# Performance work log

Measured on AMD Instinct MI355X. Metric: run time of the kernel, lower is better.

Reference implementation:

```python
import jax, jax.numpy as jnp
import numpy as np

N_NODES = 50000
N_EDGES = 800000
IN_DIM, HID_DIM, OUT_DIM = 256, 256, 128


def setup_inputs() -> dict:
    key = jax.random.key(0)
    ks = jax.random.split(key, 8)
    x1 = jax.random.normal(ks[0], (N_NODES, IN_DIM), dtype=jnp.float32)
    x2 = jax.random.normal(ks[1], (N_NODES, IN_DIM), dtype=jnp.float32)
    edge_index1 = jax.random.randint(ks[2], (2, N_EDGES), 0, N_NODES, dtype=jnp.int32)
    edge_index2 = jax.random.randint(ks[3], (2, N_EDGES), 0, N_NODES, dtype=jnp.int32)
    # GCNConv weights (Glorot-ish scaling)
    W1 = jax.random.normal(ks[4], (IN_DIM, HID_DIM), dtype=jnp.float32) / np.sqrt(IN_DIM)
    b1 = jnp.zeros((HID_DIM,), dtype=jnp.float32)
    W2 = jax.random.normal(ks[5], (HID_DIM, OUT_DIM), dtype=jnp.float32) / np.sqrt(HID_DIM)
    b2 = jnp.zeros((OUT_DIM,), dtype=jnp.float32)
    return {"x1": x1, "edge_index1": edge_index1, "x2": x2, "edge_index2": edge_index2,
            "W1": W1, "b1": b1, "W2": W2, "b2": b2}


def gcn_conv(x, src, dst, W, b, n_nodes):
    """PyG GCNConv: h = x @ W; symmetric-normalized scatter-add with self-loops; + bias."""
    h = x @ W  # [N, D_out]
    loop = jnp.arange(n_nodes, dtype=src.dtype)
    s = jnp.concatenate([src, loop])  # [E+N]
    d = jnp.concatenate([dst, loop])
    deg = jax.ops.segment_sum(jnp.ones_like(d, dtype=h.dtype), d, num_segments=n_nodes)
    dinv = jax.lax.rsqrt(jnp.maximum(deg, 1.0))  # deg >= 1 with self-loops
    norm = dinv[s] * dinv[d]  # [E+N]
    msg = h[s] * norm[:, None]  # [E+N, D_out]
    out = jax.ops.segment_sum(msg, d, num_segments=n_nodes)
    return out + b


def gcn_backbone(x, edge_index, W1, b1, W2, b2):
    src, dst = edge_index[0], edge_index[1]
    n = x.shape[0]
    h = jax.nn.relu(gcn_conv(x, src, dst, W1, b1, n))
    return gcn_conv(h, src, dst, W2, b2, n)


def reference(x1, edge_index1, x2, edge_index2, W1, b1, W2, b2):
    u = gcn_backbone(x1, edge_index1, W1, b1, W2, b2)
    v = gcn_backbone(x2, edge_index2, W1, b1, W2, b2)
    return (u, v)
```

## Files before the change

### kernel.cpp

```cpp
#include <hip/hip_runtime.h>

typedef __bf16 bf16x8 __attribute__((ext_vector_type(8)));
typedef float f32x4 __attribute__((ext_vector_type(4)));

constexpr int NN = 50000;
constexpr int NE = 800000;
constexpr int DIN = 256, DHID = 256, DOUT = 128;
constexpr int NCH = (NN + 255) / 256;

__device__ __forceinline__ unsigned short f2bf(float f) {
  unsigned u = __float_as_uint(f);
  u += 0x7fffu + ((u >> 16) & 1u);
  return (unsigned short)(u >> 16);
}
__device__ __forceinline__ float bf2f(unsigned short h) {
  return __uint_as_float(((unsigned)h) << 16);
}


__global__ void hist_kernel(const int* __restrict__ e0, const int* __restrict__ e1,
                            int* __restrict__ counts) {
  int g = blockIdx.y;
  const int* dst = (g ? e1 : e0) + NE;
  int* c = counts + g * NN;
  int i = blockIdx.x * blockDim.x + threadIdx.x;
  if (i < NE) atomicAdd(&c[dst[i]], 1);
}


__global__ __launch_bounds__(256) void scanA_kernel(const int* __restrict__ counts,
                                                    int* __restrict__ bsum) {
  int g = blockIdx.y, chunk = blockIdx.x, t = threadIdx.x;
  int i = chunk * 256 + t;
  int v = (i < NN) ? counts[g * NN + i] : 0;
  __shared__ int sh[256];
  sh[t] = v;
  __syncthreads();
  for (int off = 128; off > 0; off >>= 1) {
    if (t < off) sh[t] += sh[t + off];
    __syncthreads();
  }
  if (t == 0) bsum[g * NCH + chunk] = sh[0];
}

__global__ __launch_bounds__(256) void scanB_kernel(int* __restrict__ bsum,
                                                    int* __restrict__ rowptr) {
  int g = blockIdx.x, t = threadIdx.x;
  int v = (t < NCH) ? bsum[g * NCH + t] : 0;
  __shared__ int sh[256];
  sh[t] = v;
  __syncthreads();
  for (int off = 1; off < 256; off <<= 1) {
    int x = (t >= off) ? sh[t - off] : 0;
    __syncthreads();
    if (t >= off) sh[t] += x;
    __syncthreads();
  }
  if (t < NCH) bsum[g * NCH + t] = sh[t] - v;
  if (t == 255) rowptr[g * (NN + 1) + NN] = sh[255];
}

__global__ __launch_bounds__(256) void scanC_kernel(const int* __restrict__ counts,
                                                    const int* __restrict__ bsum,
                                                    int* __restrict__ rowptr,
                                                    int* __restrict__ cursor,
                                                    float* __restrict__ dinv) {
  int g = blockIdx.y, chunk = blockIdx.x, t = threadIdx.x;
  int i = chunk * 256 + t;
  int v = (i < NN) ? counts[g * NN + i] : 0;
  __shared__ int sh[256];
  sh[t] = v;
  __syncthreads();
  for (int off = 1; off < 256; off <<= 1) {
    int x = (t >= off) ? sh[t - off] : 0;
    __syncthreads();
    if (t >= off) sh[t] += x;
    __syncthreads();
  }
  if (i < NN) {
    int run = bsum[g * NCH + chunk] + sh[t] - v;
    rowptr[g * (NN + 1) + i] = run;
    cursor[g * NN + i] = run;
    dinv[g * NN + i] = rsqrtf((float)(v + 1));
  }
}

__global__ void scatter_kernel(const int* __restrict__ e0, const int* __restrict__ e1,
                               int* __restrict__ cursor, unsigned short* __restrict__ col) {
  int g = blockIdx.y;
  const int* e = g ? e1 : e0;
  int* cur = cursor + g * NN;
  unsigned short* cl = col + g * NE;
  int i = blockIdx.x * blockDim.x + threadIdx.x;
  if (i < NE) {
    int s = e[i], d = e[NE + i];
    int slot = atomicAdd(&cur[d], 1);
    cl[slot] = (unsigned short)s;
  }
}


__global__ void pack_kernel(const float* __restrict__ W1, const float* __restrict__ W2,
                            unsigned short* __restrict__ P1, unsigned short* __restrict__ P2) {
  int i = blockIdx.x * blockDim.x + threadIdx.x;
  constexpr int N1 = 8 * 16 * 64 * 8;
  constexpr int N2 = 8 * 8 * 64 * 8;
  if (i < N1) {
    int j = i & 7, lane = (i >> 3) & 63, grp = i >> 9;
    int nt = grp & 15, kb = grp >> 4;
    int k = kb * 32 + (lane >> 4) * 8 + j;
    int n = nt * 16 + (lane & 15);
    P1[i] = f2bf(W1[k * DHID + n]);
  } else if (i < N1 + N2) {
    int ii = i - N1;
    int j = ii & 7, lane = (ii >> 3) & 63, grp = ii >> 9;
    int nt = grp & 7, kb = grp >> 3;
    int k = kb * 32 + (lane >> 4) * 8 + j;
    int n = nt * 16 + (lane & 15);
    P2[ii] = f2bf(W2[k * DOUT + n]);
  }
}


template <int N, bool AF32>
__global__ __launch_bounds__(256) void mm_kernel(
    const void* __restrict__ A0, const void* __restrict__ A1,
    const unsigned short* __restrict__ Wp, unsigned short* __restrict__ Cb,
    const float* __restrict__ dinv, long long gstride) {
  constexpr int NT = N / 16;
  constexpr int K = 256;
  int g = blockIdx.y;
  const void* A = g ? A1 : A0;
  unsigned short* C = Cb + (size_t)g * gstride;
  const float* dv = dinv + g * NN;
  int wave = threadIdx.x >> 6, lane = threadIdx.x & 63;
  int q = lane >> 4, lm = lane & 15;
  int m0 = blockIdx.x * 64 + wave * 16;
  int row = m0 + lm;
  int rowc = min(row, NN - 1);
  f32x4 acc[NT];
#pragma unroll
  for (int nt = 0; nt < NT; nt++) acc[nt] = (f32x4){0.f, 0.f, 0.f, 0.f};
#pragma unroll
  for (int kb = 0; kb < K / 32; kb++) {
    int kc = kb * 32 + q * 8;
    bf16x8 a;
    if constexpr (AF32) {
      const float* Af = (const float*)A + (size_t)rowc * K + kc;
      const float4 v0 = *(const float4*)Af;
      const float4 v1 = *(const float4*)(Af + 4);
      a[0] = (__bf16)v0.x; a[1] = (__bf16)v0.y; a[2] = (__bf16)v0.z; a[3] = (__bf16)v0.w;
      a[4] = (__bf16)v1.x; a[5] = (__bf16)v1.y; a[6] = (__bf16)v1.z; a[7] = (__bf16)v1.w;
    } else {
      const unsigned short* Ab = (const unsigned short*)A + (size_t)rowc * K + kc;
      a = *(const bf16x8*)Ab;
    }
#pragma unroll
    for (int nt = 0; nt < NT; nt++) {
      bf16x8 b = *(const bf16x8*)(Wp + (((size_t)kb * NT + nt) * 64 + lane) * 8);
      acc[nt] = __builtin_amdgcn_mfma_f32_16x16x32_bf16(a, b, acc[nt], 0, 0, 0);
    }
  }
  float dvr[4];
#pragma unroll
  for (int r = 0; r < 4; r++) dvr[r] = dv[min(m0 + q * 4 + r, NN - 1)];
#pragma unroll
  for (int nt = 0; nt < NT; nt++) {
#pragma unroll
    for (int r = 0; r < 4; r++) {
      int grow = m0 + q * 4 + r;
      if (grow < NN) C[(size_t)grow * N + nt * 16 + lm] = f2bf(acc[nt][r] * dvr[r]);
    }
  }
}


__global__ __launch_bounds__(256) void agg1_kernel(
    const unsigned short* __restrict__ m1, unsigned short* __restrict__ a1,
    const int* __restrict__ rowptr, const unsigned short* __restrict__ col,
    const float* __restrict__ dinv, const float* __restrict__ b1) {
  int g = blockIdx.y;
  const unsigned short* H = m1 + (size_t)g * NN * DHID;
  unsigned short* O = a1 + (size_t)g * NN * DHID;
  const int* rp = rowptr + g * (NN + 1);
  const unsigned short* cl = col + (size_t)g * NE;
  const float* dv = dinv + g * NN;
  int node = blockIdx.x * 4 + (threadIdx.x >> 6);
  if (node >= NN) return;
  int lane = threadIdx.x & 63;
  ushort4 sv = *(const ushort4*)(H + (size_t)node * DHID + lane * 4);
  float a0 = bf2f(sv.x), a1v = bf2f(sv.y), a2 = bf2f(sv.z), a3 = bf2f(sv.w);
  int jb = rp[node], je = rp[node + 1];
  int j = jb;
  for (; j + 16 <= je; j += 16) {
    int s[16];
    ushort4 v[16];
#pragma unroll
    for (int u = 0; u < 16; u++) s[u] = cl[j + u];
#pragma unroll
    for (int u = 0; u < 16; u++) v[u] = *(const ushort4*)(H + (size_t)s[u] * DHID + lane * 4);
#pragma unroll
    for (int u = 0; u < 16; u++) {
      a0 += bf2f(v[u].x); a1v += bf2f(v[u].y);
      a2 += bf2f(v[u].z); a3 += bf2f(v[u].w);
    }
  }
  for (; j + 8 <= je; j += 8) {
    int s[8];
    ushort4 v[8];
#pragma unroll
    for (int u = 0; u < 8; u++) s[u] = cl[j + u];
#pragma unroll
    for (int u = 0; u < 8; u++) v[u] = *(const ushort4*)(H + (size_t)s[u] * DHID + lane * 4);
#pragma unroll
    for (int u = 0; u < 8; u++) {
      a0 += bf2f(v[u].x); a1v += bf2f(v[u].y);
      a2 += bf2f(v[u].z); a3 += bf2f(v[u].w);
    }
  }
  for (; j < je; j++) {
    int s = cl[j];
    ushort4 hv = *(const ushort4*)(H + (size_t)s * DHID + lane * 4);
    a0 += bf2f(hv.x); a1v += bf2f(hv.y);
    a2 += bf2f(hv.z); a3 += bf2f(hv.w);
  }
  float di = dv[node];
  float4 bb = *(const float4*)(b1 + lane * 4);
  a0 = fmaxf(fmaf(a0, di, bb.x), 0.f); a1v = fmaxf(fmaf(a1v, di, bb.y), 0.f);
  a2 = fmaxf(fmaf(a2, di, bb.z), 0.f); a3 = fmaxf(fmaf(a3, di, bb.w), 0.f);
  ushort4 out;
  out.x = f2bf(a0); out.y = f2bf(a1v); out.z = f2bf(a2); out.w = f2bf(a3);
  *(ushort4*)(O + (size_t)node * DHID + lane * 4) = out;
}


__global__ __launch_bounds__(256) void agg2_kernel(
    const unsigned short* __restrict__ m2, float* __restrict__ out,
    const int* __restrict__ rowptr, const unsigned short* __restrict__ col,
    const float* __restrict__ dinv, const float* __restrict__ b2) {
  int g = blockIdx.y;
  const unsigned short* H = m2 + (size_t)g * NN * DHID;
  float* O = out + (size_t)g * NN * DOUT;
  const int* rp = rowptr + g * (NN + 1);
  const unsigned short* cl = col + (size_t)g * NE;
  const float* dv = dinv + g * NN;
  int node = blockIdx.x * 4 + (threadIdx.x >> 6);
  if (node >= NN) return;
  int lane = threadIdx.x & 63;
  ushort2 sv = *(const ushort2*)(H + (size_t)node * DOUT + lane * 2);
  float a0 = bf2f(sv.x), a1v = bf2f(sv.y);
  int jb = rp[node], je = rp[node + 1];
  int j = jb;
  for (; j + 16 <= je; j += 16) {
    int s[16];
    ushort2 v[16];
#pragma unroll
    for (int u = 0; u < 16; u++) s[u] = cl[j + u];
#pragma unroll
    for (int u = 0; u < 16; u++) v[u] = *(const ushort2*)(H + (size_t)s[u] * DOUT + lane * 2);
#pragma unroll
    for (int u = 0; u < 16; u++) { a0 += bf2f(v[u].x); a1v += bf2f(v[u].y); }
  }
  for (; j + 8 <= je; j += 8) {
    int s[8];
    ushort2 v[8];
#pragma unroll
    for (int u = 0; u < 8; u++) s[u] = cl[j + u];
#pragma unroll
    for (int u = 0; u < 8; u++) v[u] = *(const ushort2*)(H + (size_t)s[u] * DOUT + lane * 2);
#pragma unroll
    for (int u = 0; u < 8; u++) { a0 += bf2f(v[u].x); a1v += bf2f(v[u].y); }
  }
  for (; j < je; j++) {
    int s = cl[j];
    ushort2 hv = *(const ushort2*)(H + (size_t)s * DOUT + lane * 2);
    a0 += bf2f(hv.x); a1v += bf2f(hv.y);
  }
  float di = dv[node];
  float2 bb = *(const float2*)(b2 + lane * 2);
  float2 res;
  res.x = fmaf(a0, di, bb.x); res.y = fmaf(a1v, di, bb.y);
  *(float2*)(O + (size_t)node * DOUT + lane * 2) = res;
}


extern "C" void kernel_launch(void* const* d_in, const int* in_sizes, int n_in,
                              void* d_out, int out_size, void* d_ws, size_t ws_size,
                              hipStream_t stream) {
  const float* x1 = (const float*)d_in[0];
  const int* e1 = (const int*)d_in[1];
  const float* x2 = (const float*)d_in[2];
  const int* e2 = (const int*)d_in[3];
  const float* W1 = (const float*)d_in[4];
  const float* b1 = (const float*)d_in[5];
  const float* W2 = (const float*)d_in[6];
  const float* b2 = (const float*)d_in[7];
  float* out = (float*)d_out;

  char* base = (char*)d_ws;
  size_t off = 0;
  auto alloc = [&](size_t bytes) -> void* {
    void* p = base + off;
    off = (off + bytes + 511) & ~(size_t)511;
    return p;
  };
  int* counts = (int*)alloc((size_t)2 * NN * 4);
  int* rowptr = (int*)alloc((size_t)2 * (NN + 1) * 4);
  int* cursor = (int*)alloc((size_t)2 * NN * 4);
  float* dinv = (float*)alloc((size_t)2 * NN * 4);
  int* bsum = (int*)alloc((size_t)2 * NCH * 4);
  unsigned short* col = (unsigned short*)alloc((size_t)2 * NE * 2);
  unsigned short* m1 = (unsigned short*)alloc((size_t)2 * NN * DHID * 2);
  unsigned short* a1 = (unsigned short*)alloc((size_t)2 * NN * DHID * 2);
  unsigned short* P1 = (unsigned short*)alloc((size_t)8 * 16 * 64 * 8 * 2);
  unsigned short* P2 = (unsigned short*)alloc((size_t)8 * 8 * 64 * 8 * 2);

  hipMemsetAsync(counts, 0, (size_t)2 * NN * 4, stream);
  hist_kernel<<<dim3((NE + 255) / 256, 2), 256, 0, stream>>>(e1, e2, counts);
  scanA_kernel<<<dim3(NCH, 2), 256, 0, stream>>>(counts, bsum);
  scanB_kernel<<<2, 256, 0, stream>>>(bsum, rowptr);
  scanC_kernel<<<dim3(NCH, 2), 256, 0, stream>>>(counts, bsum, rowptr, cursor, dinv);
  scatter_kernel<<<dim3((NE + 255) / 256, 2), 256, 0, stream>>>(e1, e2, cursor, col);
  pack_kernel<<<(98304 + 255) / 256, 256, 0, stream>>>(W1, W2, P1, P2);
  mm_kernel<DHID, true><<<dim3((NN + 63) / 64, 2), 256, 0, stream>>>(
      x1, x2, P1, m1, dinv, (long long)NN * DHID);
  agg1_kernel<<<dim3(NN / 4, 2), 256, 0, stream>>>(m1, a1, rowptr, col, dinv, b1);
  mm_kernel<DOUT, false><<<dim3((NN + 63) / 64, 2), 256, 0, stream>>>(
      a1, a1 + (size_t)NN * DHID, P2, m1, dinv, (long long)NN * DHID);
  agg2_kernel<<<dim3(NN / 4, 2), 256, 0, stream>>>(m1, out, rowptr, col, dinv, b2);
}
```

Measured before the change: 591.7 us.

## Split aggregation into feature slices with edge-parallel lanes and shuffle reduction

Replaces the two per-node gather kernels with one templated kernel. The feature dimension is split into 32-column slices, one block per slice, so a node's row is fetched by several blocks. Each wave splits into four 16-lane groups that take different edges, then combines partial sums with xor shuffles. The aim is to shrink the per-slice working set for cache locality and add parallelism across edges, at the cost of re-reading row pointers and column indices once per slice, much smaller 4-byte loads, and only a quarter of the lanes storing results.

Result: slower. 828.6 us (+40.0%).

```diff
diff --git a/kernel.cpp b/kernel.cpp
--- a/kernel.cpp
+++ b/kernel.cpp
@@ -175,112 +175,79 @@
 }
 
 
-__global__ __launch_bounds__(256) void agg1_kernel(
-    const unsigned short* __restrict__ m1, unsigned short* __restrict__ a1,
+template <int D, int NSL, bool RELU, typename OutT>
+__global__ __launch_bounds__(256) void agg_kernel(
+    const unsigned short* __restrict__ Hb, OutT* __restrict__ Ob,
     const int* __restrict__ rowptr, const unsigned short* __restrict__ col,
-    const float* __restrict__ dinv, const float* __restrict__ b1) {
-  int g = blockIdx.y;
-  const unsigned short* H = m1 + (size_t)g * NN * DHID;
-  unsigned short* O = a1 + (size_t)g * NN * DHID;
+    const float* __restrict__ dinv, const float* __restrict__ bias,
+    long long hgstride, long long ogstride) {
+  constexpr int CHUNKS = NN / 4;
+  int x = blockIdx.x;
+  int slice = x % NSL;
+  int rest = x / NSL;
+  int g = rest / CHUNKS;
+  int chunk = rest - g * CHUNKS;
+  int wave = threadIdx.x >> 6, lane = threadIdx.x & 63;
+  int eg = lane >> 4, l16 = lane & 15;
+  int node = chunk * 4 + wave;
+  const unsigned short* H = Hb + (size_t)g * hgstride;
   const int* rp = rowptr + g * (NN + 1);
   const unsigned short* cl = col + (size_t)g * NE;
-  const float* dv = dinv + g * NN;
-  int node = blockIdx.x * 4 + (threadIdx.x >> 6);
-  if (node >= NN) return;
-  int lane = threadIdx.x & 63;
-  ushort4 sv = *(const ushort4*)(H + (size_t)node * DHID + lane * 4);
-  float a0 = bf2f(sv.x), a1v = bf2f(sv.y), a2 = bf2f(sv.z), a3 = bf2f(sv.w);
+  int co = slice * 32 + l16 * 2;
   int jb = rp[node], je = rp[node + 1];
+  float acc0 = 0.f, acc1 = 0.f;
   int j = jb;
   for (; j + 16 <= je; j += 16) {
-    int s[16];
-    ushort4 v[16];
-#pragma unroll
-    for (int u = 0; u < 16; u++) s[u] = cl[j + u];
-#pragma unroll
-    for (int u = 0; u < 16; u++) v[u] = *(const ushort4*)(H + (size_t)s[u] * DHID + lane * 4);
-#pragma unroll
-    for (int u = 0; u < 16; u++) {
-      a0 += bf2f(v[u].x); a1v += bf2f(v[u].y);
-      a2 += bf2f(v[u].z); a3 += bf2f(v[u].w);
-    }
-  }
-  for (; j + 8 <= je; j += 8) {
-    int s[8];
-    ushort4 v[8];
-#pragma unroll
-    for (int u = 0; u < 8; u++) s[u] = cl[j + u];
-#pragma unroll
-    for (int u = 0; u < 8; u++) v[u] = *(const ushort4*)(H + (size_t)s[u] * DHID + lane * 4);
-#pragma unroll
-    for (int u = 0; u < 8; u++) {
-      a0 += bf2f(v[u].x); a1v += bf2f(v[u].y);
-      a2 += bf2f(v[u].z); a3 += bf2f(v[u].w);
-    }
-  }
-  for (; j < je; j++) {
-    int s = cl[j];
-    ushort4 hv = *(const ushort4*)(H + (size_t)s * DHID + lane * 4);
-    a0 += bf2f(hv.x); a1v += bf2f(hv.y);
-    a2 += bf2f(hv.z); a3 += bf2f(hv.w);
-  }
-  float di = dv[node];
-  float4 bb = *(const float4*)(b1 + lane * 4);
-  a0 = fmaxf(fmaf(a0, di, bb.x), 0.f); a1v = fmaxf(fmaf(a1v, di, bb.y), 0.f);
-  a2 = fmaxf(fmaf(a2, di, bb.z), 0.f); a3 = fmaxf(fmaf(a3, di, bb.w), 0.f);
-  ushort4 out;
-  out.x = f2bf(a0); out.y = f2bf(a1v); out.z = f2bf(a2); out.w = f2bf(a3);
-  *(ushort4*)(O + (size_t)node * DHID + lane * 4) = out;
-}
-
-
-__global__ __launch_bounds__(256) void agg2_kernel(
-    const unsigned short* __restrict__ m2, float* __restrict__ out,
-    const int* __restrict__ rowptr, const unsigned short* __restrict__ col,
-    const float* __restrict__ dinv, const float* __restrict__ b2) {
-  int g = blockIdx.y;
-  const unsigned short* H = m2 + (size_t)g * NN * DHID;
-  float* O = out + (size_t)g * NN * DOUT;
-  const int* rp = rowptr + g * (NN + 1);
-  const unsigned short* cl = col + (size_t)g * NE;
-  const float* dv = dinv + g * NN;
-  int node = blockIdx.x * 4 + (threadIdx.x >> 6);
-  if (node >= NN) return;
-  int lane = threadIdx.x & 63;
-  ushort2 sv = *(const ushort2*)(H + (size_t)node * DOUT + lane * 2);
-  float a0 = bf2f(sv.x), a1v = bf2f(sv.y);
-  int jb = rp[node], je = rp[node + 1];
-  int j = jb;
-  for (; j + 16 <= je; j += 16) {
-    int s[16];
-    ushort2 v[16];
-#pragma unroll
-    for (int u = 0; u < 16; u++) s[u] = cl[j + u];
-#pragma unroll
-    for (int u = 0; u < 16; u++) v[u] = *(const ushort2*)(H + (size_t)s[u] * DOUT + lane * 2);
-#pragma unroll
-    for (int u = 0; u < 16; u++) { a0 += bf2f(v[u].x); a1v += bf2f(v[u].y); }
-  }
-  for (; j + 8 <= je; j += 8) {
-    int s[8];
-    ushort2 v[8];
-#pragma unroll
-    for (int u = 0; u < 8; u++) s[u] = cl[j + u];
-#pragma unroll
-    for (int u = 0; u < 8; u++) v[u] = *(const ushort2*)(H + (size_t)s[u] * DOUT + lane * 2);
-#pragma unroll
-    for (int u = 0; u < 8; u++) { a0 += bf2f(v[u].x); a1v += bf2f(v[u].y); }
-  }
-  for (; j < je; j++) {
-    int s = cl[j];
-    ushort2 hv = *(const ushort2*)(H + (size_t)s * DOUT + lane * 2);
-    a0 += bf2f(hv.x); a1v += bf2f(hv.y);
-  }
-  float di = dv[node];
-  float2 bb = *(const float2*)(b2 + lane * 2);
-  float2 res;
-  res.x = fmaf(a0, di, bb.x); res.y = fmaf(a1v, di, bb.y);
-  *(float2*)(O + (size_t)node * DOUT + lane * 2) = res;
+    int s[4];
+    unsigned d[4];
+#pragma unroll
+    for (int u = 0; u < 4; u++) s[u] = cl[j + u * 4 + eg];
+#pragma unroll
+    for (int u = 0; u < 4; u++) d[u] = *(const unsigned*)(H + (size_t)s[u] * D + co);
+#pragma unroll
+    for (int u = 0; u < 4; u++) {
+      acc0 += __uint_as_float(d[u] << 16);
+      acc1 += __uint_as_float(d[u] & 0xffff0000u);
+    }
+  }
+  if (j + 8 <= je) {
+    int s0 = cl[j + eg], s1 = cl[j + 4 + eg];
+    unsigned d0 = *(const unsigned*)(H + (size_t)s0 * D + co);
+    unsigned d1 = *(const unsigned*)(H + (size_t)s1 * D + co);
+    acc0 += __uint_as_float(d0 << 16) + __uint_as_float(d1 << 16);
+    acc1 += __uint_as_float(d0 & 0xffff0000u) + __uint_as_float(d1 & 0xffff0000u);
+    j += 8;
+  }
+  if (j + 4 <= je) {
+    int s0 = cl[j + eg];
+    unsigned d0 = *(const unsigned*)(H + (size_t)s0 * D + co);
+    acc0 += __uint_as_float(d0 << 16);
+    acc1 += __uint_as_float(d0 & 0xffff0000u);
+    j += 4;
+  }
+  if (j + eg < je) {
+    int s0 = cl[j + eg];
+    unsigned d0 = *(const unsigned*)(H + (size_t)s0 * D + co);
+    acc0 += __uint_as_float(d0 << 16);
+    acc1 += __uint_as_float(d0 & 0xffff0000u);
+  }
+  acc0 += __shfl_xor(acc0, 16); acc0 += __shfl_xor(acc0, 32);
+  acc1 += __shfl_xor(acc1, 16); acc1 += __shfl_xor(acc1, 32);
+  if (eg == 0) {
+    unsigned sd = *(const unsigned*)(H + (size_t)node * D + co);
+    float di = dinv[g * NN + node];
+    float2 bb = *(const float2*)(bias + slice * 32 + l16 * 2);
+    float v0 = fmaf(acc0 + __uint_as_float(sd << 16), di, bb.x);
+    float v1 = fmaf(acc1 + __uint_as_float(sd & 0xffff0000u), di, bb.y);
+    if constexpr (RELU) { v0 = fmaxf(v0, 0.f); v1 = fmaxf(v1, 0.f); }
+    if constexpr (sizeof(OutT) == 2) {
+      unsigned p = ((unsigned)f2bf(v1) << 16) | (unsigned)f2bf(v0);
+      *(unsigned*)((unsigned short*)Ob + (size_t)g * ogstride + (size_t)node * D + co) = p;
+    } else {
+      float2 r; r.x = v0; r.y = v1;
+      *(float2*)((float*)Ob + (size_t)g * ogstride + (size_t)node * D + co) = r;
+    }
+  }
 }
 
 
@@ -324,8 +291,10 @@
   pack_kernel<<<(98304 + 255) / 256, 256, 0, stream>>>(W1, W2, P1, P2);
   mm_kernel<DHID, true><<<dim3((NN + 63) / 64, 2), 256, 0, stream>>>(
       x1, x2, P1, m1, dinv, (long long)NN * DHID);
-  agg1_kernel<<<dim3(NN / 4, 2), 256, 0, stream>>>(m1, a1, rowptr, col, dinv, b1);
+  agg_kernel<DHID, 8, true, unsigned short><<<8 * (NN / 4) * 2, 256, 0, stream>>>(
+      m1, a1, rowptr, col, dinv, b1, (long long)NN * DHID, (long long)NN * DHID);
   mm_kernel<DOUT, false><<<dim3((NN + 63) / 64, 2), 256, 0, stream>>>(
       a1, a1 + (size_t)NN * DHID, P2, m1, dinv, (long long)NN * DHID);
-  agg2_kernel<<<dim3(NN / 4, 2), 256, 0, stream>>>(m1, out, rowptr, col, dinv, b2);
-}
+  agg_kernel<DOUT, 4, false, float><<<4 * (NN / 4) * 2, 256, 0, stream>>>(
+      m1, out, rowptr, col, dinv, b2, (long long)NN * DHID, (long long)NN * DOUT);
+}
```

## Fuse layer-1 aggregation with the layer-2 matmul through shared memory

Applied to the files above, without the earlier changes.

Layer-1 neighbour aggregation now feeds the second GEMM directly. Each block aggregates 16 nodes, places the ReLU'd bf16 rows in LDS, then runs MFMA against the packed W2 to produce the scaled layer-2 messages. This removes the global write and re-read of the 256-wide intermediate activation, along with one kernel launch. In exchange each wave handles four nodes serially, so fewer independent waves are in flight during the gather, and blocks now wait at a barrier before the matmul.

After: 568.6 us. -3.9%, faster.

```diff
diff --git a/kernel.cpp b/kernel.cpp
--- a/kernel.cpp
+++ b/kernel.cpp
@@ -122,39 +122,31 @@
 }
 
 
-template <int N, bool AF32>
-__global__ __launch_bounds__(256) void mm_kernel(
-    const void* __restrict__ A0, const void* __restrict__ A1,
+__global__ __launch_bounds__(256) void mm1_kernel(
+    const float* __restrict__ A0, const float* __restrict__ A1,
     const unsigned short* __restrict__ Wp, unsigned short* __restrict__ Cb,
-    const float* __restrict__ dinv, long long gstride) {
-  constexpr int NT = N / 16;
-  constexpr int K = 256;
-  int g = blockIdx.y;
-  const void* A = g ? A1 : A0;
-  unsigned short* C = Cb + (size_t)g * gstride;
+    const float* __restrict__ dinv) {
+  constexpr int N = DHID, NT = N / 16, K = 256;
+  int g = blockIdx.y;
+  const float* A = g ? A1 : A0;
+  unsigned short* C = Cb + (size_t)g * NN * N;
   const float* dv = dinv + g * NN;
   int wave = threadIdx.x >> 6, lane = threadIdx.x & 63;
   int q = lane >> 4, lm = lane & 15;
   int m0 = blockIdx.x * 64 + wave * 16;
-  int row = m0 + lm;
-  int rowc = min(row, NN - 1);
+  int rowc = min(m0 + lm, NN - 1);
   f32x4 acc[NT];
 #pragma unroll
   for (int nt = 0; nt < NT; nt++) acc[nt] = (f32x4){0.f, 0.f, 0.f, 0.f};
 #pragma unroll
   for (int kb = 0; kb < K / 32; kb++) {
     int kc = kb * 32 + q * 8;
+    const float* Af = A + (size_t)rowc * K + kc;
+    const float4 v0 = *(const float4*)Af;
+    const float4 v1 = *(const float4*)(Af + 4);
     bf16x8 a;
-    if constexpr (AF32) {
-      const float* Af = (const float*)A + (size_t)rowc * K + kc;
-      const float4 v0 = *(const float4*)Af;
-      const float4 v1 = *(const float4*)(Af + 4);
-      a[0] = (__bf16)v0.x; a[1] = (__bf16)v0.y; a[2] = (__bf16)v0.z; a[3] = (__bf16)v0.w;
-      a[4] = (__bf16)v1.x; a[5] = (__bf16)v1.y; a[6] = (__bf16)v1.z; a[7] = (__bf16)v1.w;
-    } else {
-      const unsigned short* Ab = (const unsigned short*)A + (size_t)rowc * K + kc;
-      a = *(const bf16x8*)Ab;
-    }
+    a[0] = (__bf16)v0.x; a[1] = (__bf16)v0.y; a[2] = (__bf16)v0.z; a[3] = (__bf16)v0.w;
+    a[4] = (__bf16)v1.x; a[5] = (__bf16)v1.y; a[6] = (__bf16)v1.z; a[7] = (__bf16)v1.w;
 #pragma unroll
     for (int nt = 0; nt < NT; nt++) {
       bf16x8 b = *(const bf16x8*)(Wp + (((size_t)kb * NT + nt) * 64 + lane) * 8);
@@ -175,62 +167,94 @@
 }
 
 
-__global__ __launch_bounds__(256) void agg1_kernel(
-    const unsigned short* __restrict__ m1, unsigned short* __restrict__ a1,
-    const int* __restrict__ rowptr, const unsigned short* __restrict__ col,
-    const float* __restrict__ dinv, const float* __restrict__ b1) {
-  int g = blockIdx.y;
-  const unsigned short* H = m1 + (size_t)g * NN * DHID;
-  unsigned short* O = a1 + (size_t)g * NN * DHID;
+__global__ __launch_bounds__(256) void agg1mm2_kernel(
+    const unsigned short* __restrict__ m1b, const unsigned short* __restrict__ P2,
+    unsigned short* __restrict__ m2b, const int* __restrict__ rowptr,
+    const unsigned short* __restrict__ col, const float* __restrict__ dinv,
+    const float* __restrict__ b1) {
+  constexpr int LDW = DHID + 8;
+  __shared__ unsigned short sha[16 * LDW];
+  int g = blockIdx.y;
+  const unsigned short* H = m1b + (size_t)g * NN * DHID;
+  unsigned short* M2 = m2b + (size_t)g * NN * DOUT;
   const int* rp = rowptr + g * (NN + 1);
   const unsigned short* cl = col + (size_t)g * NE;
   const float* dv = dinv + g * NN;
-  int node = blockIdx.x * 4 + (threadIdx.x >> 6);
-  if (node >= NN) return;
-  int lane = threadIdx.x & 63;
-  ushort4 sv = *(const ushort4*)(H + (size_t)node * DHID + lane * 4);
-  float a0 = bf2f(sv.x), a1v = bf2f(sv.y), a2 = bf2f(sv.z), a3 = bf2f(sv.w);
-  int jb = rp[node], je = rp[node + 1];
-  int j = jb;
-  for (; j + 16 <= je; j += 16) {
-    int s[16];
-    ushort4 v[16];
-#pragma unroll
-    for (int u = 0; u < 16; u++) s[u] = cl[j + u];
-#pragma unroll
-    for (int u = 0; u < 16; u++) v[u] = *(const ushort4*)(H + (size_t)s[u] * DHID + lane * 4);
-#pragma unroll
-    for (int u = 0; u < 16; u++) {
-      a0 += bf2f(v[u].x); a1v += bf2f(v[u].y);
-      a2 += bf2f(v[u].z); a3 += bf2f(v[u].w);
-    }
-  }
-  for (; j + 8 <= je; j += 8) {
-    int s[8];
-    ushort4 v[8];
-#pragma unroll
-    for (int u = 0; u < 8; u++) s[u] = cl[j + u];
-#pragma unroll
-    for (int u = 0; u < 8; u++) v[u] = *(const ushort4*)(H + (size_t)s[u] * DHID + lane * 4);
-#pragma unroll
-    for (int u = 0; u < 8; u++) {
-      a0 += bf2f(v[u].x); a1v += bf2f(v[u].y);
-      a2 += bf2f(v[u].z); a3 += bf2f(v[u].w);
-    }
-  }
-  for (; j < je; j++) {
-    int s = cl[j];
-    ushort4 hv = *(const ushort4*)(H + (size_t)s * DHID + lane * 4);
-    a0 += bf2f(hv.x); a1v += bf2f(hv.y);
-    a2 += bf2f(hv.z); a3 += bf2f(hv.w);
-  }
-  float di = dv[node];
+  int wave = threadIdx.x >> 6, lane = threadIdx.x & 63;
+  int base = blockIdx.x * 16;
   float4 bb = *(const float4*)(b1 + lane * 4);
-  a0 = fmaxf(fmaf(a0, di, bb.x), 0.f); a1v = fmaxf(fmaf(a1v, di, bb.y), 0.f);
-  a2 = fmaxf(fmaf(a2, di, bb.z), 0.f); a3 = fmaxf(fmaf(a3, di, bb.w), 0.f);
-  ushort4 out;
-  out.x = f2bf(a0); out.y = f2bf(a1v); out.z = f2bf(a2); out.w = f2bf(a3);
-  *(ushort4*)(O + (size_t)node * DHID + lane * 4) = out;
+  for (int n = 0; n < 4; n++) {
+    int node = base + wave * 4 + n;
+    ushort4 sv = *(const ushort4*)(H + (size_t)node * DHID + lane * 4);
+    float a0 = bf2f(sv.x), a1v = bf2f(sv.y), a2 = bf2f(sv.z), a3 = bf2f(sv.w);
+    int jb = rp[node], je = rp[node + 1];
+    int j = jb;
+    for (; j + 16 <= je; j += 16) {
+      int s[16];
+      ushort4 v[16];
+#pragma unroll
+      for (int u = 0; u < 16; u++) s[u] = cl[j + u];
+#pragma unroll
+      for (int u = 0; u < 16; u++) v[u] = *(const ushort4*)(H + (size_t)s[u] * DHID + lane * 4);
+#pragma unroll
+      for (int u = 0; u < 16; u++) {
+        a0 += bf2f(v[u].x); a1v += bf2f(v[u].y);
+        a2 += bf2f(v[u].z); a3 += bf2f(v[u].w);
+      }
+    }
+    for (; j + 8 <= je; j += 8) {
+      int s[8];
+      ushort4 v[8];
+#pragma unroll
+      for (int u = 0; u < 8; u++) s[u] = cl[j + u];
+#pragma unroll
+      for (int u = 0; u < 8; u++) v[u] = *(const ushort4*)(H + (size_t)s[u] * DHID + lane * 4);
+#pragma unroll
+      for (int u = 0; u < 8; u++) {
+        a0 += bf2f(v[u].x); a1v += bf2f(v[u].y);
+        a2 += bf2f(v[u].z); a3 += bf2f(v[u].w);
+      }
+    }
+    for (; j < je; j++) {
+      int s = cl[j];
+      ushort4 hv = *(const ushort4*)(H + (size_t)s * DHID + lane * 4);
+      a0 += bf2f(hv.x); a1v += bf2f(hv.y);
+      a2 += bf2f(hv.z); a3 += bf2f(hv.w);
+    }
+    float di = dv[node];
+    a0 = fmaxf(fmaf(a0, di, bb.x), 0.f); a1v = fmaxf(fmaf(a1v, di, bb.y), 0.f);
+    a2 = fmaxf(fmaf(a2, di, bb.z), 0.f); a3 = fmaxf(fmaf(a3, di, bb.w), 0.f);
+    ushort4 o;
+    o.x = f2bf(a0); o.y = f2bf(a1v); o.z = f2bf(a2); o.w = f2bf(a3);
+    *(ushort4*)(sha + (wave * 4 + n) * LDW + lane * 4) = o;
+  }
+  __syncthreads();
+  int q = lane >> 4, lm = lane & 15;
+  f32x4 acc[2];
+  acc[0] = (f32x4){0.f, 0.f, 0.f, 0.f};
+  acc[1] = (f32x4){0.f, 0.f, 0.f, 0.f};
+  constexpr int NT2 = DOUT / 16;
+#pragma unroll
+  for (int kb = 0; kb < 8; kb++) {
+    bf16x8 a = *(const bf16x8*)(sha + lm * LDW + kb * 32 + q * 8);
+#pragma unroll
+    for (int t = 0; t < 2; t++) {
+      int nt = wave * 2 + t;
+      bf16x8 b = *(const bf16x8*)(P2 + (((size_t)kb * NT2 + nt) * 64 + lane) * 8);
+      acc[t] = __builtin_amdgcn_mfma_f32_16x16x32_bf16(a, b, acc[t], 0, 0, 0);
+    }
+  }
+  float dvr[4];
+#pragma unroll
+  for (int r = 0; r < 4; r++) dvr[r] = dv[base + q * 4 + r];
+#pragma unroll
+  for (int t = 0; t < 2; t++) {
+#pragma unroll
+    for (int r = 0; r < 4; r++) {
+      int node = base + q * 4 + r;
+      M2[(size_t)node * DOUT + (wave * 2 + t) * 16 + lm] = f2bf(acc[t][r] * dvr[r]);
+    }
+  }
 }
 
 
@@ -239,7 +263,7 @@
     const int* __restrict__ rowptr, const unsigned short* __restrict__ col,
     const float* __restrict__ dinv, const float* __restrict__ b2) {
   int g = blockIdx.y;
-  const unsigned short* H = m2 + (size_t)g * NN * DHID;
+  const unsigned short* H = m2 + (size_t)g * NN * DOUT;
   float* O = out + (size_t)g * NN * DOUT;
   const int* rp = rowptr + g * (NN + 1);
   const unsigned short* cl = col + (size_t)g * NE;
@@ -277,9 +301,9 @@
     a0 += bf2f(hv.x); a1v += bf2f(hv.y);
   }
   float di = dv[node];
-  float2 bb = *(const float2*)(b2 + lane * 2);
+  float2 bbv = *(const float2*)(b2 + lane * 2);
   float2 res;
-  res.x = fmaf(a0, di, bb.x); res.y = fmaf(a1v, di, bb.y);
+  res.x = fmaf(a0, di, bbv.x); res.y = fmaf(a1v, di, bbv.y);
   *(float2*)(O + (size_t)node * DOUT + lane * 2) = res;
 }
 
@@ -311,7 +335,7 @@
   int* bsum = (int*)alloc((size_t)2 * NCH * 4);
   unsigned short* col = (unsigned short*)alloc((size_t)2 * NE * 2);
   unsigned short* m1 = (unsigned short*)alloc((size_t)2 * NN * DHID * 2);
-  unsigned short* a1 = (unsigned short*)alloc((size_t)2 * NN * DHID * 2);
+  unsigned short* m2 = (unsigned short*)alloc((size_t)2 * NN * DOUT * 2);
   unsigned short* P1 = (unsigned short*)alloc((size_t)8 * 16 * 64 * 8 * 2);
   unsigned short* P2 = (unsigned short*)alloc((size_t)8 * 8 * 64 * 8 * 2);
 
@@ -322,10 +346,7 @@
   scanC_kernel<<<dim3(NCH, 2), 256, 0, stream>>>(counts, bsum, rowptr, cursor, dinv);
   scatter_kernel<<<dim3((NE + 255) / 256, 2), 256, 0, stream>>>(e1, e2, cursor, col);
   pack_kernel<<<(98304 + 255) / 256, 256, 0, stream>>>(W1, W2, P1, P2);
-  mm_kernel<DHID, true><<<dim3((NN + 63) / 64, 2), 256, 0, stream>>>(
-      x1, x2, P1, m1, dinv, (long long)NN * DHID);
-  agg1_kernel<<<dim3(NN / 4, 2), 256, 0, stream>>>(m1, a1, rowptr, col, dinv, b1);
-  mm_kernel<DOUT, false><<<dim3((NN + 63) / 64, 2), 256, 0, stream>>>(
-      a1, a1 + (size_t)NN * DHID, P2, m1, dinv, (long long)NN * DHID);
-  agg2_kernel<<<dim3(NN / 4, 2), 256, 0, stream>>>(m1, out, rowptr, col, dinv, b2);
-}
+  mm1_kernel<<<dim3((NN + 63) / 64, 2), 256, 0, stream>>>(x1, x2, P1, m1, dinv);
+  agg1mm2_kernel<<<dim3(NN / 16, 2), 256, 0, stream>>>(m1, P2, m2, rowptr, col, dinv, b1);
+  agg2_kernel<<<dim3(NN / 4, 2), 256, 0, stream>>>(m2, out, rowptr, col, dinv, b2);
+}
```
